# Kernel tuning notes

Hardware: AMD Instinct MI355X
Metric: run time of the kernel (lower is better)

## Reference

```python
import jax, jax.numpy as jnp
import numpy as np

WS = 7          # window_size
NH = 8          # num_heads
EMB = 128       # embedding_dim
HD = EMB // NH  # head_dim
SCALE = HD ** -0.5
LN_EPS = 1e-5


def setup_inputs() -> dict:
    key = jax.random.key(0)
    ks = jax.random.split(key, 5)
    B, N, C = 64, 3136, EMB  # H = W = 56
    x = jax.random.normal(ks[0], (B, N, C), dtype=jnp.float32)
    ln_gamma = jnp.ones((C,), dtype=jnp.float32)
    ln_beta = jnp.zeros((C,), dtype=jnp.float32)
    w_qkv = jax.random.normal(ks[1], (C, 3 * C), dtype=jnp.float32) * (C ** -0.5)
    b_qkv = jax.random.normal(ks[2], (3 * C,), dtype=jnp.float32) * 0.02
    w_out = jax.random.normal(ks[3], (C, C), dtype=jnp.float32) * (C ** -0.5)
    b_out = jax.random.normal(ks[4], (C,), dtype=jnp.float32) * 0.02
    return {"x": x, "ln_gamma": ln_gamma, "ln_beta": ln_beta,
            "w_qkv": w_qkv, "b_qkv": b_qkv, "w_out": w_out, "b_out": b_out}


def reference(x, ln_gamma, ln_beta, w_qkv, b_qkv, w_out, b_out):
    B, N, C = x.shape
    H = int(np.sqrt(N))  # static
    Wd = H

    # LayerNorm over last dim
    mu = jnp.mean(x, axis=-1, keepdims=True)
    var = jnp.mean(jnp.square(x - mu), axis=-1, keepdims=True)
    xn = (x - mu) * jax.lax.rsqrt(var + LN_EPS) * ln_gamma + ln_beta

    # divide windows: [B,N,C] -> [B*nWh*nWw, WS*WS, C]
    nW = H // WS
    win = xn.reshape(B, nW, WS, nW, WS, C).transpose(0, 1, 3, 2, 4, 5)
    win = win.reshape(-1, WS * WS, C)

    # QKV projection
    qkv = win @ w_qkv + b_qkv                      # [nw, 49, 3C]
    qkv = qkv.reshape(-1, WS * WS, 3, NH, HD).transpose(2, 0, 3, 1, 4)
    q, k, v = qkv[0], qkv[1], qkv[2]               # [nw, NH, 49, HD]

    scores = jnp.einsum('whqd,whkd->whqk', q, k) * SCALE
    probs = jax.nn.softmax(scores, axis=-1)
    attn = jnp.einsum('whqk,whkd->whqd', probs, v) # [nw, NH, 49, HD]
    attn = attn.transpose(0, 2, 1, 3).reshape(-1, WS * WS, C)

    out = attn @ w_out + b_out                     # [nw, 49, C]

    # merge windows -> [B, H, W, C]
    out = out.reshape(B, nW, nW, WS, WS, C).transpose(0, 1, 3, 2, 4, 5)
    return out.reshape(B, H, Wd, C)
```

## Files before the change

### kernel.cpp

```cpp
#include <hip/hip_runtime.h>

typedef float floatx4 __attribute__((ext_vector_type(4)));
typedef __bf16 bf16t;
typedef __bf16 bf16x8 __attribute__((ext_vector_type(8)));
typedef __bf16 bf16x4 __attribute__((ext_vector_type(4)));
typedef unsigned short u16t;
typedef unsigned int u32t;

static __device__ __forceinline__ u16t f2bf(float f) {
  return __builtin_bit_cast(u16t, (__bf16)f);
}
static __device__ __forceinline__ float bf2f(u16t h) {
  return __uint_as_float((u32t)h << 16);
}

#define MFMA(A, B, C) __builtin_amdgcn_mfma_f32_16x16x32_bf16((A), (B), (C), 0, 0, 0)

__global__ void pack_weights_kernel(const float* __restrict__ wqkv,
                                    const float* __restrict__ wout,
                                    u16t* __restrict__ wq_p,
                                    u16t* __restrict__ wo_p) {
  int g = blockIdx.x * blockDim.x + threadIdx.x;
  int l = g & 63;
  int s = (g >> 6) & 3;
  int n = g >> 8;
  int cl = l & 15;
  if (n < 24) {
    int kbase = 32 * s + ((l >> 4) * 8);
    int col = 16 * n + cl;
    u16t* dst = wq_p + g * 8;
#pragma unroll
    for (int j = 0; j < 8; ++j) dst[j] = f2bf(wqkv[(kbase + j) * 384 + col]);
  } else {
    int col = 16 * (n - 24) + cl;
    u16t* dst = wo_p + (g - 24 * 256) * 8;
    int rbase = 32 * s + 4 * (l >> 4);
#pragma unroll
    for (int j = 0; j < 8; ++j)
      dst[j] = f2bf(wout[(rbase + 16 * (j >> 2) + (j & 3)) * 128 + col]);
  }
}

__global__ __launch_bounds__(256)
__attribute__((amdgpu_waves_per_eu(4, 4))) void win_attn_kernel(
    const float* __restrict__ x, const float* __restrict__ gamma,
    const float* __restrict__ beta, const u16t* __restrict__ wq_p,
    const float* __restrict__ bqkv, const u16t* __restrict__ wo_p,
    const float* __restrict__ bout, float* __restrict__ out) {
  __shared__ u16t xnK[64][136];
  __shared__ u16t xv[9216];

  const int tid = threadIdx.x;
  const int lane = tid & 63;
  const int w = tid >> 6;
  const int llo = lane & 15;
  const int lhi = lane >> 4;

  const int wi = blockIdx.x;
  const int bimg = wi >> 6;
  const int widx = wi & 63;
  const int nwh = widx >> 3;
  const int nww = widx & 7;
  const int base_off = (((bimg * 56) + nwh * 7) * 56 + nww * 7) * 128;
  const float* xbase = x + base_off;

  for (int i = tid; i < 15 * 64; i += 256) {
    int r = 49 + (i >> 6), c = (i & 63) << 1;
    *(u32t*)&xnK[r][c] = 0;
    *(u32t*)&xv[r * 136 + c] = 0;
  }

  {
    const float g0 = gamma[2 * lane], g1 = gamma[2 * lane + 1];
    const float b0 = beta[2 * lane], b1 = beta[2 * lane + 1];
    for (int t = w; t < 49; t += 4) {
      int wr = t / 7, wc = t - wr * 7;
      const float* row = xbase + (wr * 56 + wc) * 128;
      float2 v = *(const float2*)(row + 2 * lane);
      float sm = v.x + v.y;
      float sq = v.x * v.x + v.y * v.y;
#pragma unroll
      for (int m = 1; m < 64; m <<= 1) {
        sm += __shfl_xor(sm, m);
        sq += __shfl_xor(sq, m);
      }
      float mean = sm * (1.f / 128.f);
      float var = sq * (1.f / 128.f) - mean * mean;
      float rs = rsqrtf(var + 1e-5f);
      float y0 = (v.x - mean) * rs * g0 + b0;
      float y1 = (v.y - mean) * rs * g1 + b1;
      u16t h0 = f2bf(y0), h1 = f2bf(y1);
      u16t l0 = f2bf(y0 - bf2f(h0)), l1 = f2bf(y1 - bf2f(h1));
      *(u32t*)&xnK[t][2 * lane] = (u32t)h0 | ((u32t)h1 << 16);
      *(u32t*)&xv[t * 136 + 2 * lane] = (u32t)l0 | ((u32t)l1 << 16);
    }
  }
  __syncthreads();

  const int rowA = 16 * w + llo;
  const int rowC = 16 * w + lhi * 4;
  const floatx4 z4 = {0.f, 0.f, 0.f, 0.f};

  bf16x8 a_hi[4], a_lo[4];
#pragma unroll
  for (int s = 0; s < 4; ++s) {
    a_hi[s] = *(const bf16x8*)&xnK[rowA][s * 32 + lhi * 8];
    a_lo[s] = *(const bf16x8*)&xv[rowA * 136 + s * 32 + lhi * 8];
  }
  __syncthreads();

#pragma unroll 2
  for (int h = 0; h < 8; ++h) {
    const u16t* pwk = wq_p + (((8 + h) * 4) * 64 + lane) * 8;
    const u16t* pwv = wq_p + (((16 + h) * 4) * 64 + lane) * 8;
    floatx4 ak = z4, av = z4;
#pragma unroll
    for (int s = 0; s < 4; ++s) {
      bf16x8 bk = *(const bf16x8*)(pwk + s * 512);
      bf16x8 bv = *(const bf16x8*)(pwv + s * 512);
      ak = MFMA(bk, a_hi[s], ak);
      ak = MFMA(bk, a_lo[s], ak);
      av = MFMA(a_hi[s], bv, av);
      av = MFMA(a_lo[s], bv, av);
    }
    float4 bk4 = *(const float4*)(bqkv + 128 + h * 16 + 4 * lhi);
    ushort4 kk;
    kk.x = f2bf(ak[0] + bk4.x);
    kk.y = f2bf(ak[1] + bk4.y);
    kk.z = f2bf(ak[2] + bk4.z);
    kk.w = f2bf(ak[3] + bk4.w);
    *(ushort4*)&xnK[16 * w + llo][h * 16 + 4 * lhi] = kk;
    float bv_ = bqkv[256 + h * 16 + llo];
    ushort4 vv;
    vv.x = f2bf(av[0] + bv_);
    vv.y = f2bf(av[1] + bv_);
    vv.z = f2bf(av[2] + bv_);
    vv.w = f2bf(av[3] + bv_);
    *(ushort4*)&xv[(h * 16 + llo) * 72 + rowC] = vv;
  }

  bf16x8 qall[8];
#pragma unroll
  for (int h = 0; h < 8; ++h) {
    const u16t* pq = wq_p + ((h * 4) * 64 + lane) * 8;
    floatx4 aq = z4;
#pragma unroll
    for (int s = 0; s < 4; ++s)
      aq = MFMA(*(const bf16x8*)(pq + s * 512), a_hi[s], aq);
    float4 bq4 = *(const float4*)(bqkv + h * 16 + 4 * lhi);
    float q0 = aq[0] + bq4.x, q1 = aq[1] + bq4.y;
    float q2 = aq[2] + bq4.z, q3 = aq[3] + bq4.w;
    qall[h][0] = (bf16t)q0;
    qall[h][1] = (bf16t)q1;
    qall[h][2] = (bf16t)q2;
    qall[h][3] = (bf16t)q3;
    qall[h][4] = (bf16t)(q0 - (float)qall[h][0]);
    qall[h][5] = (bf16t)(q1 - (float)qall[h][1]);
    qall[h][6] = (bf16t)(q2 - (float)qall[h][2]);
    qall[h][7] = (bf16t)(q3 - (float)qall[h][3]);
  }
  __syncthreads();

  bf16x4 kv4[4], vv4[4];
#pragma unroll
  for (int n = 0; n < 4; ++n)
    kv4[n] = *(const bf16x4*)&xnK[16 * n + llo][4 * lhi];
  {
    const int vrow = llo * 72;
#pragma unroll
    for (int i = 0; i < 4; ++i)
      vv4[i] = *(const bf16x4*)&xv[vrow + 16 * i + 4 * lhi];
  }

  const float SEXP = 0.25f * 1.44269504088896340736f;
  floatx4 oc[8];
#pragma unroll
  for (int n = 0; n < 8; ++n) oc[n] = z4;
  bf16x8 atf;

#pragma unroll
  for (int h = 0; h < 8; ++h) {
    floatx4 sc[4];
#pragma unroll
    for (int n = 0; n < 4; ++n) {
      bf16x8 kbf =
          __builtin_shufflevector(kv4[n], kv4[n], 0, 1, 2, 3, 0, 1, 2, 3);
      sc[n] = MFMA(kbf, qall[h], z4);
    }
    bf16x8 V0 = __builtin_shufflevector(vv4[0], vv4[1], 0, 1, 2, 3, 4, 5, 6, 7);
    bf16x8 V1 = __builtin_shufflevector(vv4[2], vv4[3], 0, 1, 2, 3, 4, 5, 6, 7);
    if (h < 7) {
      const int kcol = (h + 1) * 16 + 4 * lhi;
#pragma unroll
      for (int n = 0; n < 4; ++n)
        kv4[n] = *(const bf16x4*)&xnK[16 * n + llo][kcol];
      const int vrow = ((h + 1) * 16 + llo) * 72;
#pragma unroll
      for (int i = 0; i < 4; ++i)
        vv4[i] = *(const bf16x4*)&xv[vrow + 16 * i + 4 * lhi];
    }

    float s0 = 0.f;
#pragma unroll
    for (int n = 0; n < 4; ++n) {
#pragma unroll
      for (int j = 0; j < 4; ++j) {
        float pe;
        if (n == 3)
          pe = (4 * lhi + j < 1) ? exp2f(sc[n][j] * SEXP) : 0.f;
        else
          pe = exp2f(sc[n][j] * SEXP);
        sc[n][j] = pe;
        s0 += pe;
      }
    }
    s0 += __shfl_xor(s0, 16);
    s0 += __shfl_xor(s0, 32);
    float rq = 1.f / s0;

    bf16x8 PB0, PB1;
#pragma unroll
    for (int j = 0; j < 4; ++j) {
      PB0[j] = (bf16t)sc[0][j];
      PB0[4 + j] = (bf16t)sc[1][j];
      PB1[j] = (bf16t)sc[2][j];
      PB1[4 + j] = (bf16t)sc[3][j];
    }
    floatx4 ao = MFMA(V0, PB0, z4);
    ao = MFMA(V1, PB1, ao);
    const int hp = h & 1;
    atf[4 * hp + 0] = (bf16t)(ao[0] * rq);
    atf[4 * hp + 1] = (bf16t)(ao[1] * rq);
    atf[4 * hp + 2] = (bf16t)(ao[2] * rq);
    atf[4 * hp + 3] = (bf16t)(ao[3] * rq);

    if (hp) {
      const int p4 = h >> 1;
#pragma unroll
      for (int n = 0; n < 8; ++n)
        oc[n] = MFMA(atf,
                     *(const bf16x8*)(wo_p + ((n * 4 + p4) * 64 + lane) * 8),
                     oc[n]);
    }
  }

  float bo[8];
#pragma unroll
  for (int n = 0; n < 8; ++n) bo[n] = bout[16 * n + llo];
  float* obase = out + base_off;
#pragma unroll
  for (int r = 0; r < 4; ++r) {
    int t = rowC + r;
    if (t < 49) {
      int wr = t / 7, wc = t - wr * 7;
      float* orow = obase + (wr * 56 + wc) * 128;
#pragma unroll
      for (int n = 0; n < 8; ++n) orow[16 * n + llo] = oc[n][r] + bo[n];
    }
  }
}

extern "C" void kernel_launch(void* const* d_in, const int* in_sizes, int n_in,
                              void* d_out, int out_size, void* d_ws,
                              size_t ws_size, hipStream_t stream) {
  const float* x = (const float*)d_in[0];
  const float* ln_g = (const float*)d_in[1];
  const float* ln_b = (const float*)d_in[2];
  const float* w_qkv = (const float*)d_in[3];
  const float* b_qkv = (const float*)d_in[4];
  const float* w_out = (const float*)d_in[5];
  const float* b_out = (const float*)d_in[6];
  float* out = (float*)d_out;

  u16t* wq_p = (u16t*)d_ws;
  u16t* wo_p = wq_p + 24 * 256 * 8;

  hipLaunchKernelGGL(pack_weights_kernel, dim3(32), dim3(256), 0, stream,
                     w_qkv, w_out, wq_p, wo_p);
  hipLaunchKernelGGL(win_attn_kernel, dim3(4096), dim3(256), 0, stream, x,
                     ln_g, ln_b, wq_p, b_qkv, wo_p, b_out, out);
}
```

Before: 314.1 us.

## Drop split-bf16 Q residual, fuse softmax exp into score loop, defer output projection

Q is no longer kept as a hi/lo bf16 pair; only the rounded bf16 value is kept and duplicated across both K halves, so the score MFMA now sums the same product twice. The scale constant is halved to compensate. The exp and bf16 packing of probabilities are fused into the per-tile score loop, and the output projection MFMAs move after the head loop using all four stored attention fragments. This reduces register pressure and conversion work, at the cost of lower Q precision and less overlap of the output projection with the attention math.

```diff
diff --git a/kernel.cpp b/kernel.cpp
--- a/kernel.cpp
+++ b/kernel.cpp
@@ -139,7 +139,7 @@
     *(ushort4*)&xv[(h * 16 + llo) * 72 + rowC] = vv;
   }
 
-  bf16x8 qall[8];
+  bf16x4 qall[8];
 #pragma unroll
   for (int h = 0; h < 8; ++h) {
     const u16t* pq = wq_p + ((h * 4) * 64 + lane) * 8;
@@ -148,16 +148,10 @@
     for (int s = 0; s < 4; ++s)
       aq = MFMA(*(const bf16x8*)(pq + s * 512), a_hi[s], aq);
     float4 bq4 = *(const float4*)(bqkv + h * 16 + 4 * lhi);
-    float q0 = aq[0] + bq4.x, q1 = aq[1] + bq4.y;
-    float q2 = aq[2] + bq4.z, q3 = aq[3] + bq4.w;
-    qall[h][0] = (bf16t)q0;
-    qall[h][1] = (bf16t)q1;
-    qall[h][2] = (bf16t)q2;
-    qall[h][3] = (bf16t)q3;
-    qall[h][4] = (bf16t)(q0 - (float)qall[h][0]);
-    qall[h][5] = (bf16t)(q1 - (float)qall[h][1]);
-    qall[h][6] = (bf16t)(q2 - (float)qall[h][2]);
-    qall[h][7] = (bf16t)(q3 - (float)qall[h][3]);
+    qall[h][0] = (bf16t)(aq[0] + bq4.x);
+    qall[h][1] = (bf16t)(aq[1] + bq4.y);
+    qall[h][2] = (bf16t)(aq[2] + bq4.z);
+    qall[h][3] = (bf16t)(aq[3] + bq4.w);
   }
   __syncthreads();
 
@@ -172,20 +166,33 @@
       vv4[i] = *(const bf16x4*)&xv[vrow + 16 * i + 4 * lhi];
   }
 
-  const float SEXP = 0.25f * 1.44269504088896340736f;
-  floatx4 oc[8];
-#pragma unroll
-  for (int n = 0; n < 8; ++n) oc[n] = z4;
-  bf16x8 atf;
+  const float SEXP = 0.125f * 1.44269504088896340736f;
+  bf16x8 atf_all[4];
 
 #pragma unroll
   for (int h = 0; h < 8; ++h) {
-    floatx4 sc[4];
+    bf16x8 qfh =
+        __builtin_shufflevector(qall[h], qall[h], 0, 1, 2, 3, 0, 1, 2, 3);
+    float s0 = 0.f;
+    bf16x8 PB0, PB1;
 #pragma unroll
     for (int n = 0; n < 4; ++n) {
       bf16x8 kbf =
           __builtin_shufflevector(kv4[n], kv4[n], 0, 1, 2, 3, 0, 1, 2, 3);
-      sc[n] = MFMA(kbf, qall[h], z4);
+      floatx4 scn = MFMA(kbf, qfh, z4);
+#pragma unroll
+      for (int j = 0; j < 4; ++j) {
+        float pe;
+        if (n == 3)
+          pe = (4 * lhi + j < 1) ? exp2f(scn[j] * SEXP) : 0.f;
+        else
+          pe = exp2f(scn[j] * SEXP);
+        if (n < 2)
+          PB0[4 * n + j] = (bf16t)pe;
+        else
+          PB1[4 * (n - 2) + j] = (bf16t)pe;
+        s0 += pe;
+      }
     }
     bf16x8 V0 = __builtin_shufflevector(vv4[0], vv4[1], 0, 1, 2, 3, 4, 5, 6, 7);
     bf16x8 V1 = __builtin_shufflevector(vv4[2], vv4[3], 0, 1, 2, 3, 4, 5, 6, 7);
@@ -200,48 +207,28 @@
         vv4[i] = *(const bf16x4*)&xv[vrow + 16 * i + 4 * lhi];
     }
 
-    float s0 = 0.f;
-#pragma unroll
-    for (int n = 0; n < 4; ++n) {
-#pragma unroll
-      for (int j = 0; j < 4; ++j) {
-        float pe;
-        if (n == 3)
-          pe = (4 * lhi + j < 1) ? exp2f(sc[n][j] * SEXP) : 0.f;
-        else
-          pe = exp2f(sc[n][j] * SEXP);
-        sc[n][j] = pe;
-        s0 += pe;
-      }
-    }
     s0 += __shfl_xor(s0, 16);
     s0 += __shfl_xor(s0, 32);
     float rq = 1.f / s0;
 
-    bf16x8 PB0, PB1;
-#pragma unroll
-    for (int j = 0; j < 4; ++j) {
-      PB0[j] = (bf16t)sc[0][j];
-      PB0[4 + j] = (bf16t)sc[1][j];
-      PB1[j] = (bf16t)sc[2][j];
-      PB1[4 + j] = (bf16t)sc[3][j];
-    }
     floatx4 ao = MFMA(V0, PB0, z4);
     ao = MFMA(V1, PB1, ao);
     const int hp = h & 1;
-    atf[4 * hp + 0] = (bf16t)(ao[0] * rq);
-    atf[4 * hp + 1] = (bf16t)(ao[1] * rq);
-    atf[4 * hp + 2] = (bf16t)(ao[2] * rq);
-    atf[4 * hp + 3] = (bf16t)(ao[3] * rq);
-
-    if (hp) {
-      const int p4 = h >> 1;
-#pragma unroll
-      for (int n = 0; n < 8; ++n)
-        oc[n] = MFMA(atf,
-                     *(const bf16x8*)(wo_p + ((n * 4 + p4) * 64 + lane) * 8),
-                     oc[n]);
-    }
+#pragma unroll
+    for (int r = 0; r < 4; ++r)
+      atf_all[h >> 1][4 * hp + r] = (bf16t)(ao[r] * rq);
+  }
+
+  floatx4 oc[8];
+#pragma unroll
+  for (int n = 0; n < 8; ++n) oc[n] = z4;
+#pragma unroll
+  for (int p4 = 0; p4 < 4; ++p4) {
+#pragma unroll
+    for (int n = 0; n < 8; ++n)
+      oc[n] = MFMA(atf_all[p4],
+                   *(const bf16x8*)(wo_p + ((n * 4 + p4) * 64 + lane) * 8),
+                   oc[n]);
   }
 
   float bo[8];
```

Result: no change. 313.6 us (-0.1%).
